# Kernel optimization log

Hardware: AMD Instinct MI355X
Metric: run time of the kernel (lower is better)

## Reference

```python
import jax, jax.numpy as jnp
import numpy as np

B, T, N, D = 256, 200, 8, 64
MODEL = N * D          # 512
FFN_H = 1024 * N // 4  # 2048
EPS = 1.1920929e-07    # torch.finfo(float32).eps (nn.RMSNorm default eps=None)


def setup_inputs() -> dict:
    key = jax.random.key(0)
    ks = jax.random.split(key, 9)
    def xavier(k, shape):
        fan_in, fan_out = shape[-2], shape[-1]
        lim = float(np.sqrt(6.0 / (fan_in + fan_out)))
        return jax.random.uniform(k, shape, jnp.float32, -lim, lim)
    q = jax.random.normal(ks[0], (B, N, D), jnp.float32)
    seq = jax.random.normal(ks[1], (B, T, MODEL), jnp.float32)
    seq_mask = jax.random.randint(ks[2], (B, T), 0, 2) > 0
    seq_mask = seq_mask.at[:, 0].set(True)  # ensure >=1 valid position per row
    return {
        "q": q,
        "seq": seq,
        "rms_w": jnp.ones((MODEL,), jnp.float32),
        "w1": xavier(ks[3], (MODEL, FFN_H)),
        "w2": xavier(ks[4], (MODEL, FFN_H)),
        "w3": xavier(ks[5], (FFN_H, MODEL)),
        "w_k": xavier(ks[6], (N, D, D)),
        "w_v": xavier(ks[7], (N, D, D)),
        "seq_mask": seq_mask,
    }


def reference(q, seq, rms_w, w1, w2, w3, w_k, w_v, seq_mask):
    # RMSNorm
    sn = seq * jax.lax.rsqrt(jnp.mean(seq * seq, axis=-1, keepdims=True) + EPS) * rms_w
    # SwiGLU FFN + residual (dropout=0 / eval)
    h = (jax.nn.silu(sn @ w1) * (sn @ w2)) @ w3 + seq  # (B,T,N*D)
    hh = h.reshape(B, T, N, D)
    keys = jnp.einsum('btnd,nde->bnte', hh, w_k)    # (B,N,T,D)
    values = jnp.einsum('btnd,nde->bnte', hh, w_v)  # (B,N,T,D)
    scale = D ** (-0.5)
    scores = jnp.einsum('bnd,bntd->bnt', q, keys) * scale  # single-query attention
    scores = jnp.where(seq_mask[:, None, :], scores, -jnp.inf)
    attn = jax.nn.softmax(scores, axis=-1)
    ctx = jnp.einsum('bnt,bntd->bnd', attn, values)
    return ctx + q
```

## Files before the change

### kernel.cpp

```cpp
#include <hip/hip_runtime.h>
#include <hip/hip_fp16.h>
#include <cstdint>
#include <cstddef>

typedef unsigned short u16t;
typedef __bf16 bf16x8 __attribute__((ext_vector_type(8)));
typedef float f32x4 __attribute__((ext_vector_type(4)));
typedef unsigned short u16x8 __attribute__((ext_vector_type(8)));

#define BT_ROWS 51200
#define MODEL 512
#define FFNH 2048

__device__ __forceinline__ float bf2f(u16t u) {
  union { unsigned int i; float f; } v; v.i = ((unsigned int)u) << 16; return v.f;
}
__device__ __forceinline__ u16t f2bf(float f) {
  union { float f; unsigned int i; } v; v.f = f;
  return (u16t)((v.i + 0x7fffu + ((v.i >> 16) & 1u)) >> 16);
}
__device__ __forceinline__ float ldf(const void* p, size_t i, int dt) {
  if (dt == 1) return ((const float*)p)[i];
  u16t u = ((const u16t*)p)[i];
  if (dt == 0) return bf2f(u);
  __half h; *(u16t*)&h = u; return __half2float(h);
}
__device__ __forceinline__ void stf(void* p, size_t i, int dt, float f) {
  if (dt == 1) { ((float*)p)[i] = f; }
  else if (dt == 0) { ((u16t*)p)[i] = f2bf(f); }
  else { __half h = __float2half(f); ((u16t*)p)[i] = *(u16t*)&h; }
}
__device__ __forceinline__ void gl2lds16(const void* g, void* l) {
  __builtin_amdgcn_global_load_lds((const __attribute__((address_space(1))) void*)g,
                                   (__attribute__((address_space(3))) void*)l, 16, 0, 0);
}

__global__ __launch_bounds__(256) void detect_dtype_k(const unsigned int* __restrict__ w1,
                                                      int* __restrict__ dflag) {
  __shared__ int sh[8];
  int a = 0, bc = 0;
  for (int it = 0; it < 64; it++) {
    unsigned int w = w1[it * 256 + threadIdx.x];
    u16t lo = (u16t)(w & 0xffffu), hi = (u16t)(w >> 16);
    float flo = bf2f(lo);
    a += (!(fabsf(flo) < 0.25f)) ? 1 : 0;
    __half hh; *(u16t*)&hh = hi; float fhi = __half2float(hh);
    bc += (fabsf(fhi) > 0.25f && fabsf(fhi) < 256.f) ? 1 : 0;
  }
#pragma unroll
  for (int o = 32; o; o >>= 1) { a += __shfl_xor(a, o); bc += __shfl_xor(bc, o); }
  int w = threadIdx.x >> 6;
  if ((threadIdx.x & 63) == 0) { sh[w] = a; sh[4 + w] = bc; }
  __syncthreads();
  if (threadIdx.x == 0) {
    int A = sh[0] + sh[1] + sh[2] + sh[3];
    int B = sh[4] + sh[5] + sh[6] + sh[7];
    dflag[0] = (A > 256) ? 1 : ((B < 256) ? 2 : 0);
  }
}

__global__ __launch_bounds__(256) void detect_mask_k(const unsigned int* __restrict__ msk,
                                                     int* __restrict__ flag) {
  int i = blockIdx.x * 256 + threadIdx.x;
  int bad = 0;
  if (i < 12800) bad = (msk[i] > 1u) ? 1 : 0;
  unsigned long long bl = __ballot(bad);
  if ((threadIdx.x & 63) == 0 && bl) atomicOr(flag, 1);
}

__global__ __launch_bounds__(256) void rmsnorm_k(const void* __restrict__ seq,
                                                 const void* __restrict__ w,
                                                 const int* __restrict__ dfp,
                                                 u16t* __restrict__ xn) {
  const int dt = dfp[0];
  int row = blockIdx.x * 4 + (threadIdx.x >> 6);
  int lane = threadIdx.x & 63;
  size_t base = (size_t)row * MODEL + lane * 8;
  float x[8]; float ss = 0.f;
  if (dt == 0) {
    u16x8 xv = *(const u16x8*)((const u16t*)seq + base);
#pragma unroll
    for (int j = 0; j < 8; j++) { x[j] = bf2f(xv[j]); ss += x[j] * x[j]; }
  } else if (dt == 1) {
    const f32x4* p = (const f32x4*)((const float*)seq + base);
    f32x4 va = p[0], vb = p[1];
#pragma unroll
    for (int j = 0; j < 4; j++) { x[j] = va[j]; x[4 + j] = vb[j]; }
#pragma unroll
    for (int j = 0; j < 8; j++) ss += x[j] * x[j];
  } else {
#pragma unroll
    for (int j = 0; j < 8; j++) { x[j] = ldf(seq, base + j, dt); ss += x[j] * x[j]; }
  }
#pragma unroll
  for (int o = 32; o; o >>= 1) ss += __shfl_xor(ss, o);
  float rstd = rsqrtf(ss * (1.f / 512.f) + 1.1920929e-07f);
  u16x8 ov;
#pragma unroll
  for (int j = 0; j < 8; j++) ov[j] = f2bf(x[j] * rstd * ldf(w, lane * 8 + j, dt));
  *(u16x8*)(xn + base) = ov;
}

__global__ __launch_bounds__(256) void transpose_k(const void* __restrict__ src,
                                                   u16t* __restrict__ dst,
                                                   const int* __restrict__ dfp,
                                                   int R, int C) {
  const int dt = dfp[0];
  __shared__ u16t tile[32][33];
  int x = threadIdx.x & 31, y = threadIdx.x >> 5;
  int c0 = blockIdx.x * 32, r0 = blockIdx.y * 32;
#pragma unroll
  for (int i = 0; i < 32; i += 8)
    tile[y + i][x] = f2bf(ldf(src, (size_t)(r0 + y + i) * C + c0 + x, dt));
  __syncthreads();
#pragma unroll
  for (int i = 0; i < 32; i += 8) dst[(size_t)(c0 + y + i) * R + r0 + x] = tile[x][y + i];
}


__global__ __launch_bounds__(256, 4) void ffn_gemm1(const u16t* __restrict__ Xn,
                                                    const u16t* __restrict__ W1t,
                                                    const u16t* __restrict__ W2t,
                                                    u16t* __restrict__ Act) {
  __shared__ u16t As[128 * 64];
  __shared__ u16t B1s[64 * 64];
  __shared__ u16t B2s[64 * 64];
  const int tid = threadIdx.x;
  const int lane = tid & 63;
  const int wave = tid >> 6;
  const int wr = wave >> 1, wc = wave & 1;
  const int quad = lane >> 4, l16 = lane & 15;
  const int nBase = blockIdx.x * 64;
  const int mBase = blockIdx.y * 128;
  const int wuBase = tid & ~63;

  f32x4 acc1[4][2], acc2[4][2];
  const f32x4 zf = {0.f, 0.f, 0.f, 0.f};
#pragma unroll
  for (int i = 0; i < 4; i++)
#pragma unroll
    for (int j = 0; j < 2; j++) { acc1[i][j] = zf; acc2[i][j] = zf; }

  for (int kt = 0; kt < MODEL; kt += 64) {
#pragma unroll
    for (int c = 0; c < 4; c++) {
      int chunk = c * 256 + tid;
      int r = chunk >> 3, k8 = (chunk & 7) ^ (r & 7);
      gl2lds16(Xn + (size_t)(mBase + r) * MODEL + kt + k8 * 8, As + (size_t)(c * 256 + wuBase) * 8);
    }
#pragma unroll
    for (int c = 0; c < 2; c++) {
      int chunk = c * 256 + tid;
      int r = chunk >> 3, k8 = (chunk & 7) ^ (r & 7);
      gl2lds16(W1t + (size_t)(nBase + r) * MODEL + kt + k8 * 8, B1s + (size_t)(c * 256 + wuBase) * 8);
      gl2lds16(W2t + (size_t)(nBase + r) * MODEL + kt + k8 * 8, B2s + (size_t)(c * 256 + wuBase) * 8);
    }
    __syncthreads();
#pragma unroll
    for (int ks = 0; ks < 64; ks += 32) {
      bf16x8 a[4], b1[2], b2[2];
      const int sw = (ks >> 3) + quad;
#pragma unroll
      for (int mi = 0; mi < 4; mi++) {
        int row = wr * 64 + mi * 16 + l16;
        a[mi] = *(const bf16x8*)(As + row * 64 + ((sw ^ (row & 7)) << 3));
      }
#pragma unroll
      for (int ni = 0; ni < 2; ni++) {
        int row = wc * 32 + ni * 16 + l16;
        b1[ni] = *(const bf16x8*)(B1s + row * 64 + ((sw ^ (row & 7)) << 3));
        b2[ni] = *(const bf16x8*)(B2s + row * 64 + ((sw ^ (row & 7)) << 3));
      }
#pragma unroll
      for (int mi = 0; mi < 4; mi++)
#pragma unroll
        for (int ni = 0; ni < 2; ni++) {
          acc1[mi][ni] = __builtin_amdgcn_mfma_f32_16x16x32_bf16(a[mi], b1[ni], acc1[mi][ni], 0, 0, 0);
          acc2[mi][ni] = __builtin_amdgcn_mfma_f32_16x16x32_bf16(a[mi], b2[ni], acc2[mi][ni], 0, 0, 0);
        }
    }
    __syncthreads();
  }
#pragma unroll
  for (int mi = 0; mi < 4; mi++)
#pragma unroll
    for (int ni = 0; ni < 2; ni++)
#pragma unroll
      for (int r = 0; r < 4; r++) {
        int row = mBase + wr * 64 + mi * 16 + quad * 4 + r;
        int col = nBase + wc * 32 + ni * 16 + l16;
        float g1 = acc1[mi][ni][r], g2 = acc2[mi][ni][r];
        float sl = g1 / (1.f + __expf(-g1));
        Act[(size_t)row * FFNH + col] = f2bf(sl * g2);
      }
}

__global__ __launch_bounds__(256, 4) void ffn_gemm2(const u16t* __restrict__ Act,
                                                    const u16t* __restrict__ W3t,
                                                    const void* __restrict__ Seq,
                                                    const int* __restrict__ dfp,
                                                    u16t* __restrict__ H, int rowOff) {
  __shared__ u16t As[128 * 64];
  __shared__ u16t Bs[128 * 64];
  const int dt = dfp[0];
  const int tid = threadIdx.x;
  const int lane = tid & 63;
  const int wave = tid >> 6;
  const int wr = wave >> 1, wc = wave & 1;
  const int quad = lane >> 4, l16 = lane & 15;
  const int nBase = blockIdx.x * 128;
  const int mBase = blockIdx.y * 128;
  const int wuBase = tid & ~63;

  f32x4 acc[4][4];
  const f32x4 zf = {0.f, 0.f, 0.f, 0.f};
#pragma unroll
  for (int i = 0; i < 4; i++)
#pragma unroll
    for (int j = 0; j < 4; j++) acc[i][j] = zf;

  for (int kt = 0; kt < FFNH; kt += 64) {
#pragma unroll
    for (int c = 0; c < 4; c++) {
      int chunk = c * 256 + tid;
      int r = chunk >> 3, k8 = (chunk & 7) ^ (r & 7);
      gl2lds16(Act + (size_t)(mBase + r) * FFNH + kt + k8 * 8, As + (size_t)(c * 256 + wuBase) * 8);
      gl2lds16(W3t + (size_t)(nBase + r) * FFNH + kt + k8 * 8, Bs + (size_t)(c * 256 + wuBase) * 8);
    }
    __syncthreads();
#pragma unroll
    for (int ks = 0; ks < 64; ks += 32) {
      bf16x8 a[4], b[4];
      const int sw = (ks >> 3) + quad;
#pragma unroll
      for (int mi = 0; mi < 4; mi++) {
        int row = wr * 64 + mi * 16 + l16;
        a[mi] = *(const bf16x8*)(As + row * 64 + ((sw ^ (row & 7)) << 3));
      }
#pragma unroll
      for (int ni = 0; ni < 4; ni++) {
        int row = wc * 64 + ni * 16 + l16;
        b[ni] = *(const bf16x8*)(Bs + row * 64 + ((sw ^ (row & 7)) << 3));
      }
#pragma unroll
      for (int mi = 0; mi < 4; mi++)
#pragma unroll
        for (int ni = 0; ni < 4; ni++)
          acc[mi][ni] = __builtin_amdgcn_mfma_f32_16x16x32_bf16(a[mi], b[ni], acc[mi][ni], 0, 0, 0);
    }
    __syncthreads();
  }
#pragma unroll
  for (int mi = 0; mi < 4; mi++)
#pragma unroll
    for (int ni = 0; ni < 4; ni++)
#pragma unroll
      for (int r = 0; r < 4; r++) {
        int grow = rowOff + mBase + wr * 64 + mi * 16 + quad * 4 + r;
        int col = nBase + wc * 64 + ni * 16 + l16;
        float v = acc[mi][ni][r] + ldf(Seq, (size_t)grow * MODEL + col, dt);
        H[(size_t)grow * MODEL + col] = f2bf(v);
      }
}

__global__ __launch_bounds__(256) void attn_k(const u16t* __restrict__ H,
                                              const void* __restrict__ q,
                                              const void* __restrict__ wk,
                                              const void* __restrict__ wv,
                                              const int* __restrict__ mask,
                                              const int* __restrict__ mflagp,
                                              const int* __restrict__ dfp,
                                              void* __restrict__ out) {
  const int b = blockIdx.x >> 3;
  const int n = blockIdx.x & 7;
  const int tid = threadIdx.x;
  const int w = tid >> 6;
  const int lane = tid & 63;
  const int T = 200;
  const int HS = 66;
  const int dt = dfp[0];
  const int mflag = mflagp[0];

  __shared__ u16t hbuf[200 * HS];
  __shared__ float qk[64];
  __shared__ float sc[200];
  __shared__ float part[256];
  __shared__ float red[8];
  __shared__ float ctx[64];

  for (int chunk = tid; chunk < 1600; chunk += 256) {
    int r = chunk >> 3, c = (chunk & 7) << 3;
    u16x8 v = *(const u16x8*)(H + (size_t)(b * 200 + r) * MODEL + n * 64 + c);
#pragma unroll
    for (int j = 0; j < 8; j++) hbuf[r * HS + c + j] = v[j];
  }

  {
    int d = tid >> 2, sub = tid & 3;
    float s = 0.f;
    size_t wb = ((size_t)n * 64 + d) * 64 + sub * 16;
    size_t qb = (size_t)(b * 8 + n) * 64 + sub * 16;
#pragma unroll
    for (int i = 0; i < 16; i++) s += ldf(wk, wb + i, dt) * ldf(q, qb + i, dt);
    part[tid] = s;
  }
  __syncthreads();
  if (tid < 64) qk[tid] = part[tid * 4] + part[tid * 4 + 1] + part[tid * 4 + 2] + part[tid * 4 + 3];
  __syncthreads();

  float sv = -INFINITY;
  if (tid < T) {
    float s = 0.f;
#pragma unroll 16
    for (int d = 0; d < 64; d++) s += bf2f(hbuf[tid * HS + d]) * qk[d];
    int mv = mflag ? (int)((const unsigned char*)mask)[b * 200 + tid] : mask[b * 200 + tid];
    sv = mv ? s * 0.125f : -INFINITY;
  }

  float mx = sv;
#pragma unroll
  for (int o = 32; o; o >>= 1) mx = fmaxf(mx, __shfl_xor(mx, o));
  if (lane == 0) red[w] = mx;
  __syncthreads();
  float gmax = fmaxf(fmaxf(red[0], red[1]), fmaxf(red[2], red[3]));
  float e = 0.f;
  if (gmax == -INFINITY) {
    if (tid == 0) e = 1.f;
  } else if (tid < T) {
    e = __expf(sv - gmax);
  }
  float s = e;
#pragma unroll
  for (int o = 32; o; o >>= 1) s += __shfl_xor(s, o);
  if (lane == 0) red[4 + w] = s;
  __syncthreads();
  float inv = 1.f / (red[4] + red[5] + red[6] + red[7]);
  if (tid < T) sc[tid] = e * inv;
  __syncthreads();

  float a2 = 0.f;
  for (int t = w; t < T; t += 4) a2 += sc[t] * bf2f(hbuf[t * HS + lane]);
  part[tid] = a2;
  __syncthreads();
  if (tid < 64) ctx[tid] = part[tid] + part[64 + tid] + part[128 + tid] + part[192 + tid];
  __syncthreads();

  {
    int od = tid & 63;
    float s2 = 0.f;
#pragma unroll
    for (int i = 0; i < 16; i++) {
      int d = w * 16 + i;
      s2 += ctx[d] * ldf(wv, ((size_t)n * 64 + d) * 64 + od, dt);
    }
    part[tid] = s2;
  }
  __syncthreads();
  if (tid < 64) {
    size_t oi = (size_t)(b * 8 + n) * 64 + tid;
    stf(out, oi, dt,
        part[tid] + part[64 + tid] + part[128 + tid] + part[192 + tid] + ldf(q, oi, dt));
  }
}

extern "C" void kernel_launch(void* const* d_in, const int* in_sizes, int n_in,
                              void* d_out, int out_size, void* d_ws, size_t ws_size,
                              hipStream_t stream) {
  (void)in_sizes; (void)n_in; (void)out_size;
  const void* q   = d_in[0];
  const void* seq = d_in[1];
  const void* rw  = d_in[2];
  const void* w1  = d_in[3];
  const void* w2  = d_in[4];
  const void* w3  = d_in[5];
  const void* wk  = d_in[6];
  const void* wv  = d_in[7];
  const int*  msk = (const int*)d_in[8];

  char* ws = (char*)d_ws;
  size_t off = 0;
  auto alloc = [&](size_t b) { void* p = ws + off; off = (off + b + 255) & ~(size_t)255; return p; };
  int*  flags = (int*)alloc(512);
  int*  mflag = flags + 0;
  int*  dflag = flags + 4;
  u16t* Xn  = (u16t*)alloc((size_t)BT_ROWS * MODEL * 2);
  u16t* W1t = (u16t*)alloc((size_t)FFNH * MODEL * 2);
  u16t* W2t = (u16t*)alloc((size_t)FFNH * MODEL * 2);
  u16t* W3t = (u16t*)alloc((size_t)MODEL * FFNH * 2);
  size_t actBytes = (ws_size > off) ? (ws_size - off) : 0;
  long tpc = (long)(actBytes / ((size_t)128 * FFNH * 2));
  if (tpc < 1) tpc = 1;
  if (tpc > 200) tpc = 200;
  u16t* ActB = (u16t*)(ws + off);

  hipMemsetAsync(flags, 0, 512, stream);
  detect_dtype_k<<<dim3(1), dim3(256), 0, stream>>>((const unsigned int*)w1, dflag);
  detect_mask_k<<<dim3(50), dim3(256), 0, stream>>>((const unsigned int*)msk, mflag);

  rmsnorm_k<<<dim3(BT_ROWS / 4), dim3(256), 0, stream>>>(seq, rw, dflag, Xn);
  transpose_k<<<dim3(FFNH / 32, MODEL / 32), dim3(256), 0, stream>>>(w1, W1t, dflag, MODEL, FFNH);
  transpose_k<<<dim3(FFNH / 32, MODEL / 32), dim3(256), 0, stream>>>(w2, W2t, dflag, MODEL, FFNH);
  transpose_k<<<dim3(MODEL / 32, FFNH / 32), dim3(256), 0, stream>>>(w3, W3t, dflag, FFNH, MODEL);

  for (int t0 = 0; t0 < 400; t0 += (int)tpc) {
    int tiles = (400 - t0 < (int)tpc) ? (400 - t0) : (int)tpc;
    int rows0 = t0 * 128;
    ffn_gemm1<<<dim3(FFNH / 64, tiles), dim3(256), 0, stream>>>(
        Xn + (size_t)rows0 * MODEL, W1t, W2t, ActB);
    ffn_gemm2<<<dim3(MODEL / 128, tiles), dim3(256), 0, stream>>>(
        ActB, W3t, seq, dflag, Xn, rows0);
  }
  attn_k<<<dim3(2048), dim3(256), 0, stream>>>(Xn, q, wk, wv, msk, mflag, dflag, d_out);
}
```

Baseline: 693.5 us.

## Rewrite FFN GEMMs as 256x256 tiles with software-pipelined LDS double buffering

Both FFN GEMMs move from 128-row tiles on 256 threads to 256x256 tiles on 512 threads. A shared gemm256_core double-buffers the LDS stages and interleaves global-to-LDS loads with MFMA quarter-blocks, using explicit vmcnt waits, sched barriers and setprio. W1 and W2 are transposed into one interleaved buffer so a single B tile carries matching gate and up columns for the SwiGLU epilogue, and block indices are swizzled across XCDs for L2 locality. This targets LDS/global traffic and barrier stalls, at the cost of higher register and LDS pressure and fewer resident blocks per CU.

```diff
diff --git a/kernel.cpp b/kernel.cpp
--- a/kernel.cpp
+++ b/kernel.cpp
@@ -104,7 +104,7 @@
 __global__ __launch_bounds__(256) void transpose_k(const void* __restrict__ src,
                                                    u16t* __restrict__ dst,
                                                    const int* __restrict__ dfp,
-                                                   int R, int C) {
+                                                   int R, int C, int ih) {
   const int dt = dfp[0];
   __shared__ u16t tile[32][33];
   int x = threadIdx.x & 31, y = threadIdx.x >> 5;
@@ -114,150 +114,203 @@
     tile[y + i][x] = f2bf(ldf(src, (size_t)(r0 + y + i) * C + c0 + x, dt));
   __syncthreads();
 #pragma unroll
-  for (int i = 0; i < 32; i += 8) dst[(size_t)(c0 + y + i) * R + r0 + x] = tile[x][y + i];
-}
-
-
-__global__ __launch_bounds__(256, 4) void ffn_gemm1(const u16t* __restrict__ Xn,
-                                                    const u16t* __restrict__ W1t,
-                                                    const u16t* __restrict__ W2t,
-                                                    u16t* __restrict__ Act) {
-  __shared__ u16t As[128 * 64];
-  __shared__ u16t B1s[64 * 64];
-  __shared__ u16t B2s[64 * 64];
+  for (int i = 0; i < 32; i += 8) {
+    int n = c0 + y + i;
+    int vr = (ih >= 0) ? (((n >> 4) << 5) + ih * 16 + (n & 15)) : n;
+    dst[(size_t)vr * R + r0 + x] = tile[x][y + i];
+  }
+}
+
+
+#define FENCE_BAR()                              \
+  do {                                           \
+    __builtin_amdgcn_sched_barrier(0);           \
+    __builtin_amdgcn_s_barrier();                \
+    __builtin_amdgcn_sched_barrier(0);           \
+  } while (0)
+
+#define MM16(afr, bfr, MHc, NHc)                                                    \
+  do {                                                                              \
+    __builtin_amdgcn_s_setprio(1);                                                  \
+    _Pragma("unroll") for (int ks_ = 0; ks_ < 2; ks_++)                             \
+        _Pragma("unroll") for (int mi_ = 0; mi_ < 4; mi_++)                         \
+            _Pragma("unroll") for (int ni_ = 0; ni_ < 2; ni_++)                     \
+                acc[(MHc)*4 + mi_][(NHc)*2 + ni_] =                                 \
+                    __builtin_amdgcn_mfma_f32_16x16x32_bf16(                        \
+                        afr[mi_][ks_], bfr[ni_][ks_],                               \
+                        acc[(MHc)*4 + mi_][(NHc)*2 + ni_], 0, 0, 0);                \
+    __builtin_amdgcn_s_setprio(0);                                                  \
+  } while (0)
+
+template <int K>
+__device__ __forceinline__ void gemm256_core(const u16t* __restrict__ Ag,
+                                             const u16t* __restrict__ Bg,
+                                             u16t* __restrict__ As,
+                                             u16t* __restrict__ Bs,
+                                             f32x4 (&acc)[8][4]) {
+  constexpr int NKT = K / 64;
   const int tid = threadIdx.x;
   const int lane = tid & 63;
   const int wave = tid >> 6;
-  const int wr = wave >> 1, wc = wave & 1;
+  const int wr = wave >> 2, wc = wave & 3;
   const int quad = lane >> 4, l16 = lane & 15;
-  const int nBase = blockIdx.x * 64;
-  const int mBase = blockIdx.y * 128;
-  const int wuBase = tid & ~63;
-
-  f32x4 acc1[4][2], acc2[4][2];
+  const int wu = tid & ~63;
+
+  auto stage = [&](const u16t* __restrict__ G, u16t* __restrict__ L, int s, int h) {
+#pragma unroll
+    for (int c = 0; c < 2; c++) {
+      int chunk = c * 512 + tid;
+      int r = chunk >> 3;
+      int k8 = (chunk & 7) ^ (r & 7);
+      gl2lds16(G + (size_t)(h * 128 + r) * K + s * 64 + k8 * 8,
+               L + (s & 1) * 16384 + h * 8192 + (size_t)(c * 512 + wu) * 8);
+    }
+  };
+  auto lda = [&](bf16x8(&a)[4][2], int u, int MH) {
+    const u16t* S = As + (u & 1) * 16384;
+#pragma unroll
+    for (int ks = 0; ks < 2; ks++)
+#pragma unroll
+      for (int mi = 0; mi < 4; mi++) {
+        int row = wr * 128 + MH * 64 + mi * 16 + l16;
+        int sw = (ks * 4 + quad) ^ (row & 7);
+        a[mi][ks] = *(const bf16x8*)(S + row * 64 + sw * 8);
+      }
+  };
+  auto ldb = [&](bf16x8(&b)[2][2], int u, int NH) {
+    const u16t* S = Bs + (u & 1) * 16384;
+#pragma unroll
+    for (int ks = 0; ks < 2; ks++)
+#pragma unroll
+      for (int ni = 0; ni < 2; ni++) {
+        int row = wc * 64 + NH * 32 + ni * 16 + l16;
+        int sw = (ks * 4 + quad) ^ (row & 7);
+        b[ni][ks] = *(const bf16x8*)(S + row * 64 + sw * 8);
+      }
+  };
+
+  bf16x8 a[4][2], b0[2][2], b1[2][2];
+
+  stage(Ag, As, 0, 0);
+  stage(Ag, As, 0, 1);
+  stage(Bg, Bs, 0, 0);
+  stage(Bg, Bs, 0, 1);
+  if (NKT > 1) stage(Ag, As, 1, 0);
+  __builtin_amdgcn_sched_barrier(0);
+  if (NKT > 1) asm volatile("s_waitcnt vmcnt(2)" ::: "memory");
+  else         asm volatile("s_waitcnt vmcnt(0)" ::: "memory");
+  __builtin_amdgcn_s_barrier();
+  __builtin_amdgcn_sched_barrier(0);
+
+  for (int u = 0; u < NKT; u++) {
+    lda(a, u, 0);
+    ldb(b0, u, 0);
+    if (u + 1 < NKT) stage(Ag, As, u + 1, 1);
+    FENCE_BAR();
+    MM16(a, b0, 0, 0);
+    FENCE_BAR();
+    ldb(b1, u, 1);
+    if (u + 1 < NKT) stage(Bg, Bs, u + 1, 0);
+    FENCE_BAR();
+    MM16(a, b1, 0, 1);
+    FENCE_BAR();
+    lda(a, u, 1);
+    if (u + 1 < NKT) stage(Bg, Bs, u + 1, 1);
+    FENCE_BAR();
+    MM16(a, b0, 1, 0);
+    FENCE_BAR();
+    if (u + 2 < NKT) stage(Ag, As, u + 2, 0);
+    FENCE_BAR();
+    MM16(a, b1, 1, 1);
+    __builtin_amdgcn_sched_barrier(0);
+    if (u < NKT - 2)       asm volatile("s_waitcnt vmcnt(2)" ::: "memory");
+    else if (u == NKT - 2) asm volatile("s_waitcnt vmcnt(0)" ::: "memory");
+    __builtin_amdgcn_s_barrier();
+    __builtin_amdgcn_sched_barrier(0);
+  }
+}
+
+__device__ __forceinline__ int xcd_swz(int o, int nwg) {
+  int q = nwg >> 3, r = nwg & 7;
+  int xcd = o & 7, i = o >> 3;
+  return (xcd < r ? xcd * (q + 1) : r * (q + 1) + (xcd - r) * q) + i;
+}
+
+__global__ __launch_bounds__(512, 2) void ffn_gemm1(const u16t* __restrict__ Xn,
+                                                    const u16t* __restrict__ W12t,
+                                                    u16t* __restrict__ Act) {
+  __shared__ u16t As[2 * 16384];
+  __shared__ u16t Bs[2 * 16384];
+  const int tid = threadIdx.x;
+  const int lane = tid & 63;
+  const int wave = tid >> 6;
+  const int wr = wave >> 2, wc = wave & 3;
+  const int quad = lane >> 4, l16 = lane & 15;
+
+  int o = blockIdx.y * 16 + blockIdx.x;
+  int s = xcd_swz(o, gridDim.y * 16);
+  int bx = s & 15, by = s >> 4;
+
+  f32x4 acc[8][4];
   const f32x4 zf = {0.f, 0.f, 0.f, 0.f};
 #pragma unroll
-  for (int i = 0; i < 4; i++)
-#pragma unroll
-    for (int j = 0; j < 2; j++) { acc1[i][j] = zf; acc2[i][j] = zf; }
-
-  for (int kt = 0; kt < MODEL; kt += 64) {
-#pragma unroll
-    for (int c = 0; c < 4; c++) {
-      int chunk = c * 256 + tid;
-      int r = chunk >> 3, k8 = (chunk & 7) ^ (r & 7);
-      gl2lds16(Xn + (size_t)(mBase + r) * MODEL + kt + k8 * 8, As + (size_t)(c * 256 + wuBase) * 8);
-    }
-#pragma unroll
-    for (int c = 0; c < 2; c++) {
-      int chunk = c * 256 + tid;
-      int r = chunk >> 3, k8 = (chunk & 7) ^ (r & 7);
-      gl2lds16(W1t + (size_t)(nBase + r) * MODEL + kt + k8 * 8, B1s + (size_t)(c * 256 + wuBase) * 8);
-      gl2lds16(W2t + (size_t)(nBase + r) * MODEL + kt + k8 * 8, B2s + (size_t)(c * 256 + wuBase) * 8);
-    }
-    __syncthreads();
-#pragma unroll
-    for (int ks = 0; ks < 64; ks += 32) {
-      bf16x8 a[4], b1[2], b2[2];
-      const int sw = (ks >> 3) + quad;
-#pragma unroll
-      for (int mi = 0; mi < 4; mi++) {
-        int row = wr * 64 + mi * 16 + l16;
-        a[mi] = *(const bf16x8*)(As + row * 64 + ((sw ^ (row & 7)) << 3));
-      }
-#pragma unroll
-      for (int ni = 0; ni < 2; ni++) {
-        int row = wc * 32 + ni * 16 + l16;
-        b1[ni] = *(const bf16x8*)(B1s + row * 64 + ((sw ^ (row & 7)) << 3));
-        b2[ni] = *(const bf16x8*)(B2s + row * 64 + ((sw ^ (row & 7)) << 3));
-      }
-#pragma unroll
-      for (int mi = 0; mi < 4; mi++)
-#pragma unroll
-        for (int ni = 0; ni < 2; ni++) {
-          acc1[mi][ni] = __builtin_amdgcn_mfma_f32_16x16x32_bf16(a[mi], b1[ni], acc1[mi][ni], 0, 0, 0);
-          acc2[mi][ni] = __builtin_amdgcn_mfma_f32_16x16x32_bf16(a[mi], b2[ni], acc2[mi][ni], 0, 0, 0);
-        }
-    }
-    __syncthreads();
-  }
-#pragma unroll
-  for (int mi = 0; mi < 4; mi++)
-#pragma unroll
-    for (int ni = 0; ni < 2; ni++)
+  for (int m = 0; m < 8; m++)
+#pragma unroll
+    for (int n = 0; n < 4; n++) acc[m][n] = zf;
+
+  gemm256_core<512>(Xn + (size_t)by * 256 * 512, W12t + (size_t)bx * 256 * 512, As, Bs, acc);
+
+  const int mBase = by * 256;
+#pragma unroll
+  for (int mi = 0; mi < 8; mi++)
+#pragma unroll
+    for (int p = 0; p < 2; p++)
 #pragma unroll
       for (int r = 0; r < 4; r++) {
-        int row = mBase + wr * 64 + mi * 16 + quad * 4 + r;
-        int col = nBase + wc * 32 + ni * 16 + l16;
-        float g1 = acc1[mi][ni][r], g2 = acc2[mi][ni][r];
+        int row = mBase + wr * 128 + mi * 16 + quad * 4 + r;
+        int col = bx * 128 + (wc * 2 + p) * 16 + l16;
+        float g1 = acc[mi][2 * p][r], g2 = acc[mi][2 * p + 1][r];
         float sl = g1 / (1.f + __expf(-g1));
         Act[(size_t)row * FFNH + col] = f2bf(sl * g2);
       }
 }
 
-__global__ __launch_bounds__(256, 4) void ffn_gemm2(const u16t* __restrict__ Act,
+__global__ __launch_bounds__(512, 2) void ffn_gemm2(const u16t* __restrict__ Act,
                                                     const u16t* __restrict__ W3t,
                                                     const void* __restrict__ Seq,
                                                     const int* __restrict__ dfp,
                                                     u16t* __restrict__ H, int rowOff) {
-  __shared__ u16t As[128 * 64];
-  __shared__ u16t Bs[128 * 64];
+  __shared__ u16t As[2 * 16384];
+  __shared__ u16t Bs[2 * 16384];
   const int dt = dfp[0];
   const int tid = threadIdx.x;
   const int lane = tid & 63;
   const int wave = tid >> 6;
-  const int wr = wave >> 1, wc = wave & 1;
+  const int wr = wave >> 2, wc = wave & 3;
   const int quad = lane >> 4, l16 = lane & 15;
-  const int nBase = blockIdx.x * 128;
-  const int mBase = blockIdx.y * 128;
-  const int wuBase = tid & ~63;
-
-  f32x4 acc[4][4];
+
+  int o = blockIdx.y * 2 + blockIdx.x;
+  int s = xcd_swz(o, gridDim.y * 2);
+  int bx = s & 1, by = s >> 1;
+
+  f32x4 acc[8][4];
   const f32x4 zf = {0.f, 0.f, 0.f, 0.f};
 #pragma unroll
-  for (int i = 0; i < 4; i++)
-#pragma unroll
-    for (int j = 0; j < 4; j++) acc[i][j] = zf;
-
-  for (int kt = 0; kt < FFNH; kt += 64) {
-#pragma unroll
-    for (int c = 0; c < 4; c++) {
-      int chunk = c * 256 + tid;
-      int r = chunk >> 3, k8 = (chunk & 7) ^ (r & 7);
-      gl2lds16(Act + (size_t)(mBase + r) * FFNH + kt + k8 * 8, As + (size_t)(c * 256 + wuBase) * 8);
-      gl2lds16(W3t + (size_t)(nBase + r) * FFNH + kt + k8 * 8, Bs + (size_t)(c * 256 + wuBase) * 8);
-    }
-    __syncthreads();
-#pragma unroll
-    for (int ks = 0; ks < 64; ks += 32) {
-      bf16x8 a[4], b[4];
-      const int sw = (ks >> 3) + quad;
-#pragma unroll
-      for (int mi = 0; mi < 4; mi++) {
-        int row = wr * 64 + mi * 16 + l16;
-        a[mi] = *(const bf16x8*)(As + row * 64 + ((sw ^ (row & 7)) << 3));
-      }
-#pragma unroll
-      for (int ni = 0; ni < 4; ni++) {
-        int row = wc * 64 + ni * 16 + l16;
-        b[ni] = *(const bf16x8*)(Bs + row * 64 + ((sw ^ (row & 7)) << 3));
-      }
-#pragma unroll
-      for (int mi = 0; mi < 4; mi++)
-#pragma unroll
-        for (int ni = 0; ni < 4; ni++)
-          acc[mi][ni] = __builtin_amdgcn_mfma_f32_16x16x32_bf16(a[mi], b[ni], acc[mi][ni], 0, 0, 0);
-    }
-    __syncthreads();
-  }
-#pragma unroll
-  for (int mi = 0; mi < 4; mi++)
+  for (int m = 0; m < 8; m++)
+#pragma unroll
+    for (int n = 0; n < 4; n++) acc[m][n] = zf;
+
+  gemm256_core<2048>(Act + (size_t)by * 256 * 2048, W3t + (size_t)bx * 256 * 2048, As, Bs, acc);
+
+  const int mBase = by * 256;
+#pragma unroll
+  for (int mi = 0; mi < 8; mi++)
 #pragma unroll
     for (int ni = 0; ni < 4; ni++)
 #pragma unroll
       for (int r = 0; r < 4; r++) {
-        int grow = rowOff + mBase + wr * 64 + mi * 16 + quad * 4 + r;
-        int col = nBase + wc * 64 + ni * 16 + l16;
+        int grow = rowOff + mBase + wr * 128 + mi * 16 + quad * 4 + r;
+        int col = bx * 256 + wc * 64 + ni * 16 + l16;
         float v = acc[mi][ni][r] + ldf(Seq, (size_t)grow * MODEL + col, dt);
         H[(size_t)grow * MODEL + col] = f2bf(v);
       }
@@ -383,14 +436,13 @@
   int*  flags = (int*)alloc(512);
   int*  mflag = flags + 0;
   int*  dflag = flags + 4;
-  u16t* Xn  = (u16t*)alloc((size_t)BT_ROWS * MODEL * 2);
-  u16t* W1t = (u16t*)alloc((size_t)FFNH * MODEL * 2);
-  u16t* W2t = (u16t*)alloc((size_t)FFNH * MODEL * 2);
-  u16t* W3t = (u16t*)alloc((size_t)MODEL * FFNH * 2);
+  u16t* Xn   = (u16t*)alloc((size_t)BT_ROWS * MODEL * 2);
+  u16t* W12t = (u16t*)alloc((size_t)2 * FFNH * MODEL * 2);
+  u16t* W3t  = (u16t*)alloc((size_t)MODEL * FFNH * 2);
   size_t actBytes = (ws_size > off) ? (ws_size - off) : 0;
-  long tpc = (long)(actBytes / ((size_t)128 * FFNH * 2));
-  if (tpc < 1) tpc = 1;
-  if (tpc > 200) tpc = 200;
+  long ppc = (long)(actBytes / ((size_t)256 * FFNH * 2));
+  if (ppc < 1) ppc = 1;
+  if (ppc > 100) ppc = 100;
   u16t* ActB = (u16t*)(ws + off);
 
   hipMemsetAsync(flags, 0, 512, stream);
@@ -398,16 +450,16 @@
   detect_mask_k<<<dim3(50), dim3(256), 0, stream>>>((const unsigned int*)msk, mflag);
 
   rmsnorm_k<<<dim3(BT_ROWS / 4), dim3(256), 0, stream>>>(seq, rw, dflag, Xn);
-  transpose_k<<<dim3(FFNH / 32, MODEL / 32), dim3(256), 0, stream>>>(w1, W1t, dflag, MODEL, FFNH);
-  transpose_k<<<dim3(FFNH / 32, MODEL / 32), dim3(256), 0, stream>>>(w2, W2t, dflag, MODEL, FFNH);
-  transpose_k<<<dim3(MODEL / 32, FFNH / 32), dim3(256), 0, stream>>>(w3, W3t, dflag, FFNH, MODEL);
-
-  for (int t0 = 0; t0 < 400; t0 += (int)tpc) {
-    int tiles = (400 - t0 < (int)tpc) ? (400 - t0) : (int)tpc;
-    int rows0 = t0 * 128;
-    ffn_gemm1<<<dim3(FFNH / 64, tiles), dim3(256), 0, stream>>>(
-        Xn + (size_t)rows0 * MODEL, W1t, W2t, ActB);
-    ffn_gemm2<<<dim3(MODEL / 128, tiles), dim3(256), 0, stream>>>(
+  transpose_k<<<dim3(FFNH / 32, MODEL / 32), dim3(256), 0, stream>>>(w1, W12t, dflag, MODEL, FFNH, 0);
+  transpose_k<<<dim3(FFNH / 32, MODEL / 32), dim3(256), 0, stream>>>(w2, W12t, dflag, MODEL, FFNH, 1);
+  transpose_k<<<dim3(MODEL / 32, FFNH / 32), dim3(256), 0, stream>>>(w3, W3t, dflag, FFNH, MODEL, -1);
+
+  for (int p0 = 0; p0 < 200; p0 += (int)ppc) {
+    int panels = (200 - p0 < (int)ppc) ? (200 - p0) : (int)ppc;
+    int rows0 = p0 * 256;
+    ffn_gemm1<<<dim3(16, panels), dim3(512), 0, stream>>>(
+        Xn + (size_t)rows0 * MODEL, W12t, ActB);
+    ffn_gemm2<<<dim3(2, panels), dim3(512), 0, stream>>>(
         ActB, W3t, seq, dflag, Xn, rows0);
   }
   attn_k<<<dim3(2048), dim3(256), 0, stream>>>(Xn, q, wk, wv, msk, mflag, dflag, d_out);
```

After: 774.7 us. 1.12x slower.

## Stage gemm1 epilogue through LDS and widen gemm2 tiles to 128x256

Applied to the files above, without the earlier changes.

The first FFN GEMM now writes its SiLU-gated output into shared memory and then stores it with 16-byte vectorised global writes, instead of scattered 2-byte stores. The second GEMM doubles its output tile width to 256 columns, with each wave owning a 128x64 sub-tile. This halves the grid and the number of times the activation tiles are reloaded. The cost is more accumulators per thread and lower occupancy (launch bounds 2 instead of 4), which could hurt latency hiding.

```diff
diff --git a/kernel.cpp b/kernel.cpp
--- a/kernel.cpp
+++ b/kernel.cpp
@@ -122,9 +122,10 @@
                                                     const u16t* __restrict__ W1t,
                                                     const u16t* __restrict__ W2t,
                                                     u16t* __restrict__ Act) {
-  __shared__ u16t As[128 * 64];
-  __shared__ u16t B1s[64 * 64];
-  __shared__ u16t B2s[64 * 64];
+  __shared__ u16t shs[16384];
+  u16t* As  = shs;
+  u16t* B1s = shs + 8192;
+  u16t* B2s = shs + 12288;
   const int tid = threadIdx.x;
   const int lane = tid & 63;
   const int wave = tid >> 6;
@@ -187,35 +188,42 @@
     for (int ni = 0; ni < 2; ni++)
 #pragma unroll
       for (int r = 0; r < 4; r++) {
-        int row = mBase + wr * 64 + mi * 16 + quad * 4 + r;
-        int col = nBase + wc * 32 + ni * 16 + l16;
+        int rl = wr * 64 + mi * 16 + quad * 4 + r;
+        int cl = wc * 32 + ni * 16 + l16;
         float g1 = acc1[mi][ni][r], g2 = acc2[mi][ni][r];
         float sl = g1 / (1.f + __expf(-g1));
-        Act[(size_t)row * FFNH + col] = f2bf(sl * g2);
-      }
-}
-
-__global__ __launch_bounds__(256, 4) void ffn_gemm2(const u16t* __restrict__ Act,
+        shs[rl * 72 + cl] = f2bf(sl * g2);
+      }
+  __syncthreads();
+  {
+    int row = tid >> 1, half = tid & 1;
+    const u16t* sp = shs + row * 72 + half * 32;
+    u16t* gp = Act + (size_t)(mBase + row) * FFNH + nBase + half * 32;
+#pragma unroll
+    for (int j = 0; j < 4; j++) *(u16x8*)(gp + j * 8) = *(const u16x8*)(sp + j * 8);
+  }
+}
+
+__global__ __launch_bounds__(256, 2) void ffn_gemm2(const u16t* __restrict__ Act,
                                                     const u16t* __restrict__ W3t,
                                                     const void* __restrict__ Seq,
                                                     const int* __restrict__ dfp,
                                                     u16t* __restrict__ H, int rowOff) {
   __shared__ u16t As[128 * 64];
-  __shared__ u16t Bs[128 * 64];
+  __shared__ u16t Bs[256 * 64];
   const int dt = dfp[0];
   const int tid = threadIdx.x;
   const int lane = tid & 63;
-  const int wave = tid >> 6;
-  const int wr = wave >> 1, wc = wave & 1;
+  const int wc = tid >> 6;
   const int quad = lane >> 4, l16 = lane & 15;
-  const int nBase = blockIdx.x * 128;
+  const int nBase = blockIdx.x * 256;
   const int mBase = blockIdx.y * 128;
   const int wuBase = tid & ~63;
 
-  f32x4 acc[4][4];
+  f32x4 acc[8][4];
   const f32x4 zf = {0.f, 0.f, 0.f, 0.f};
 #pragma unroll
-  for (int i = 0; i < 4; i++)
+  for (int i = 0; i < 8; i++)
 #pragma unroll
     for (int j = 0; j < 4; j++) acc[i][j] = zf;
 
@@ -225,16 +233,21 @@
       int chunk = c * 256 + tid;
       int r = chunk >> 3, k8 = (chunk & 7) ^ (r & 7);
       gl2lds16(Act + (size_t)(mBase + r) * FFNH + kt + k8 * 8, As + (size_t)(c * 256 + wuBase) * 8);
+    }
+#pragma unroll
+    for (int c = 0; c < 8; c++) {
+      int chunk = c * 256 + tid;
+      int r = chunk >> 3, k8 = (chunk & 7) ^ (r & 7);
       gl2lds16(W3t + (size_t)(nBase + r) * FFNH + kt + k8 * 8, Bs + (size_t)(c * 256 + wuBase) * 8);
     }
     __syncthreads();
 #pragma unroll
     for (int ks = 0; ks < 64; ks += 32) {
-      bf16x8 a[4], b[4];
+      bf16x8 a[8], b[4];
       const int sw = (ks >> 3) + quad;
 #pragma unroll
-      for (int mi = 0; mi < 4; mi++) {
-        int row = wr * 64 + mi * 16 + l16;
+      for (int mi = 0; mi < 8; mi++) {
+        int row = mi * 16 + l16;
         a[mi] = *(const bf16x8*)(As + row * 64 + ((sw ^ (row & 7)) << 3));
       }
 #pragma unroll
@@ -243,7 +256,7 @@
         b[ni] = *(const bf16x8*)(Bs + row * 64 + ((sw ^ (row & 7)) << 3));
       }
 #pragma unroll
-      for (int mi = 0; mi < 4; mi++)
+      for (int mi = 0; mi < 8; mi++)
 #pragma unroll
         for (int ni = 0; ni < 4; ni++)
           acc[mi][ni] = __builtin_amdgcn_mfma_f32_16x16x32_bf16(a[mi], b[ni], acc[mi][ni], 0, 0, 0);
@@ -251,12 +264,12 @@
     __syncthreads();
   }
 #pragma unroll
-  for (int mi = 0; mi < 4; mi++)
+  for (int mi = 0; mi < 8; mi++)
 #pragma unroll
     for (int ni = 0; ni < 4; ni++)
 #pragma unroll
       for (int r = 0; r < 4; r++) {
-        int grow = rowOff + mBase + wr * 64 + mi * 16 + quad * 4 + r;
+        int grow = rowOff + mBase + mi * 16 + quad * 4 + r;
         int col = nBase + wc * 64 + ni * 16 + l16;
         float v = acc[mi][ni][r] + ldf(Seq, (size_t)grow * MODEL + col, dt);
         H[(size_t)grow * MODEL + col] = f2bf(v);
@@ -407,7 +420,7 @@
     int rows0 = t0 * 128;
     ffn_gemm1<<<dim3(FFNH / 64, tiles), dim3(256), 0, stream>>>(
         Xn + (size_t)rows0 * MODEL, W1t, W2t, ActB);
-    ffn_gemm2<<<dim3(MODEL / 128, tiles), dim3(256), 0, stream>>>(
+    ffn_gemm2<<<dim3(MODEL / 256, tiles), dim3(256), 0, stream>>>(
         ActB, W3t, seq, dflag, Xn, rows0);
   }
   attn_k<<<dim3(2048), dim3(256), 0, stream>>>(Xn, q, wk, wv, msk, mflag, dflag, d_out);
```

Result: slower. 738.6 us (+6.5%).

## Inline dtype detection, merge weight transposes, and swizzle GEMM block order

Applied to the files above, without the earlier changes.

Removes the separate dtype-detect kernel and memset by having each kernel detect the dtype from a wavefront-wide ballot over 64 words of w1. The mask check is collapsed to a single block, and the three transpose launches become one. A block-index swizzle is added to both FFN GEMMs to improve cache locality. Together these aim to cut launch count and serialization overhead. The risk is that the reduced dtype-detection sample is less robust than the original heuristic.

```diff
diff --git a/kernel.cpp b/kernel.cpp
--- a/kernel.cpp
+++ b/kernel.cpp
@@ -35,44 +35,46 @@
                                    (__attribute__((address_space(3))) void*)l, 16, 0, 0);
 }
 
-__global__ __launch_bounds__(256) void detect_dtype_k(const unsigned int* __restrict__ w1,
-                                                      int* __restrict__ dflag) {
-  __shared__ int sh[8];
-  int a = 0, bc = 0;
-  for (int it = 0; it < 64; it++) {
-    unsigned int w = w1[it * 256 + threadIdx.x];
-    u16t lo = (u16t)(w & 0xffffu), hi = (u16t)(w >> 16);
-    float flo = bf2f(lo);
-    a += (!(fabsf(flo) < 0.25f)) ? 1 : 0;
-    __half hh; *(u16t*)&hh = hi; float fhi = __half2float(hh);
-    bc += (fabsf(fhi) > 0.25f && fabsf(fhi) < 256.f) ? 1 : 0;
-  }
-#pragma unroll
-  for (int o = 32; o; o >>= 1) { a += __shfl_xor(a, o); bc += __shfl_xor(bc, o); }
-  int w = threadIdx.x >> 6;
-  if ((threadIdx.x & 63) == 0) { sh[w] = a; sh[4 + w] = bc; }
-  __syncthreads();
-  if (threadIdx.x == 0) {
-    int A = sh[0] + sh[1] + sh[2] + sh[3];
-    int B = sh[4] + sh[5] + sh[6] + sh[7];
-    dflag[0] = (A > 256) ? 1 : ((B < 256) ? 2 : 0);
-  }
+__device__ __forceinline__ int detect_dt_inline(const unsigned int* __restrict__ w1p) {
+  int lane = threadIdx.x & 63;
+  unsigned int w = w1p[lane];
+  u16t lo = (u16t)(w & 0xffffu), hi = (u16t)(w >> 16);
+  float flo = bf2f(lo);
+  __half hh; *(u16t*)&hh = hi; float fhi = __half2float(hh);
+  int afire = (!(fabsf(flo) < 0.25f)) ? 1 : 0;
+  int bfire = (fabsf(fhi) > 0.25f && fabsf(fhi) < 256.f) ? 1 : 0;
+  int A = __popcll(__ballot(afire));
+  int B = __popcll(__ballot(bfire));
+  return (A > 16) ? 1 : ((B < 16) ? 2 : 0);
+}
+
+__device__ __forceinline__ void swz_xy(int& bx, int& by, const int NX) {
+  int NY = gridDim.y;
+  if ((NY & 3) != 0) return;
+  int lid = by * NX + bx;
+  int k = lid & 7, j = lid >> 3;
+  const int hx = NX >> 1;
+  bx = (k & 1) * hx + (j % hx);
+  by = (k >> 1) * (NY >> 2) + (j / hx);
 }
 
 __global__ __launch_bounds__(256) void detect_mask_k(const unsigned int* __restrict__ msk,
                                                      int* __restrict__ flag) {
-  int i = blockIdx.x * 256 + threadIdx.x;
+  __shared__ int sh[4];
   int bad = 0;
-  if (i < 12800) bad = (msk[i] > 1u) ? 1 : 0;
+  for (int it = 0; it < 50; it++) bad |= (msk[it * 256 + threadIdx.x] > 1u) ? 1 : 0;
   unsigned long long bl = __ballot(bad);
-  if ((threadIdx.x & 63) == 0 && bl) atomicOr(flag, 1);
+  int w = threadIdx.x >> 6;
+  if ((threadIdx.x & 63) == 0) sh[w] = (bl != 0ull) ? 1 : 0;
+  __syncthreads();
+  if (threadIdx.x == 0) flag[0] = sh[0] | sh[1] | sh[2] | sh[3];
 }
 
 __global__ __launch_bounds__(256) void rmsnorm_k(const void* __restrict__ seq,
                                                  const void* __restrict__ w,
-                                                 const int* __restrict__ dfp,
+                                                 const unsigned int* __restrict__ w1p,
                                                  u16t* __restrict__ xn) {
-  const int dt = dfp[0];
+  const int dt = detect_dt_inline(w1p);
   int row = blockIdx.x * 4 + (threadIdx.x >> 6);
   int lane = threadIdx.x & 63;
   size_t base = (size_t)row * MODEL + lane * 8;
@@ -101,14 +103,21 @@
   *(u16x8*)(xn + base) = ov;
 }
 
-__global__ __launch_bounds__(256) void transpose_k(const void* __restrict__ src,
-                                                   u16t* __restrict__ dst,
-                                                   const int* __restrict__ dfp,
-                                                   int R, int C) {
-  const int dt = dfp[0];
+__global__ __launch_bounds__(256) void transpose3_k(const void* __restrict__ w1,
+                                                    const void* __restrict__ w2,
+                                                    const void* __restrict__ w3,
+                                                    u16t* __restrict__ W1t,
+                                                    u16t* __restrict__ W2t,
+                                                    u16t* __restrict__ W3t) {
+  const int dt = detect_dt_inline((const unsigned int*)w1);
   __shared__ u16t tile[32][33];
+  int bid = blockIdx.x;
+  const void* src; u16t* dst; int R, C, bx, by;
+  if (bid < 1024)      { src = w1; dst = W1t; R = MODEL; C = FFNH; bx = bid & 63; by = bid >> 6; }
+  else if (bid < 2048) { int t = bid - 1024; src = w2; dst = W2t; R = MODEL; C = FFNH; bx = t & 63; by = t >> 6; }
+  else                 { int t = bid - 2048; src = w3; dst = W3t; R = FFNH; C = MODEL; bx = t & 15; by = t >> 4; }
   int x = threadIdx.x & 31, y = threadIdx.x >> 5;
-  int c0 = blockIdx.x * 32, r0 = blockIdx.y * 32;
+  int c0 = bx * 32, r0 = by * 32;
 #pragma unroll
   for (int i = 0; i < 32; i += 8)
     tile[y + i][x] = f2bf(ldf(src, (size_t)(r0 + y + i) * C + c0 + x, dt));
@@ -130,8 +139,10 @@
   const int wave = tid >> 6;
   const int wr = wave >> 1, wc = wave & 1;
   const int quad = lane >> 4, l16 = lane & 15;
-  const int nBase = blockIdx.x * 64;
-  const int mBase = blockIdx.y * 128;
+  int bx = blockIdx.x, by = blockIdx.y;
+  swz_xy(bx, by, 32);
+  const int nBase = bx * 64;
+  const int mBase = by * 128;
   const int wuBase = tid & ~63;
 
   f32x4 acc1[4][2], acc2[4][2];
@@ -198,18 +209,20 @@
 __global__ __launch_bounds__(256, 4) void ffn_gemm2(const u16t* __restrict__ Act,
                                                     const u16t* __restrict__ W3t,
                                                     const void* __restrict__ Seq,
-                                                    const int* __restrict__ dfp,
+                                                    const unsigned int* __restrict__ w1p,
                                                     u16t* __restrict__ H, int rowOff) {
   __shared__ u16t As[128 * 64];
   __shared__ u16t Bs[128 * 64];
-  const int dt = dfp[0];
+  const int dt = detect_dt_inline(w1p);
   const int tid = threadIdx.x;
   const int lane = tid & 63;
   const int wave = tid >> 6;
   const int wr = wave >> 1, wc = wave & 1;
   const int quad = lane >> 4, l16 = lane & 15;
-  const int nBase = blockIdx.x * 128;
-  const int mBase = blockIdx.y * 128;
+  int bx = blockIdx.x, by = blockIdx.y;
+  swz_xy(bx, by, 4);
+  const int nBase = bx * 128;
+  const int mBase = by * 128;
   const int wuBase = tid & ~63;
 
   f32x4 acc[4][4];
@@ -269,7 +282,7 @@
                                               const void* __restrict__ wv,
                                               const int* __restrict__ mask,
                                               const int* __restrict__ mflagp,
-                                              const int* __restrict__ dfp,
+                                              const unsigned int* __restrict__ w1p,
                                               void* __restrict__ out) {
   const int b = blockIdx.x >> 3;
   const int n = blockIdx.x & 7;
@@ -278,7 +291,7 @@
   const int lane = tid & 63;
   const int T = 200;
   const int HS = 66;
-  const int dt = dfp[0];
+  const int dt = detect_dt_inline(w1p);
   const int mflag = mflagp[0];
 
   __shared__ u16t hbuf[200 * HS];
@@ -382,7 +395,6 @@
   auto alloc = [&](size_t b) { void* p = ws + off; off = (off + b + 255) & ~(size_t)255; return p; };
   int*  flags = (int*)alloc(512);
   int*  mflag = flags + 0;
-  int*  dflag = flags + 4;
   u16t* Xn  = (u16t*)alloc((size_t)BT_ROWS * MODEL * 2);
   u16t* W1t = (u16t*)alloc((size_t)FFNH * MODEL * 2);
   u16t* W2t = (u16t*)alloc((size_t)FFNH * MODEL * 2);
@@ -393,14 +405,9 @@
   if (tpc > 200) tpc = 200;
   u16t* ActB = (u16t*)(ws + off);
 
-  hipMemsetAsync(flags, 0, 512, stream);
-  detect_dtype_k<<<dim3(1), dim3(256), 0, stream>>>((const unsigned int*)w1, dflag);
-  detect_mask_k<<<dim3(50), dim3(256), 0, stream>>>((const unsigned int*)msk, mflag);
-
-  rmsnorm_k<<<dim3(BT_ROWS / 4), dim3(256), 0, stream>>>(seq, rw, dflag, Xn);
-  transpose_k<<<dim3(FFNH / 32, MODEL / 32), dim3(256), 0, stream>>>(w1, W1t, dflag, MODEL, FFNH);
-  transpose_k<<<dim3(FFNH / 32, MODEL / 32), dim3(256), 0, stream>>>(w2, W2t, dflag, MODEL, FFNH);
-  transpose_k<<<dim3(MODEL / 32, FFNH / 32), dim3(256), 0, stream>>>(w3, W3t, dflag, FFNH, MODEL);
+  detect_mask_k<<<dim3(1), dim3(256), 0, stream>>>((const unsigned int*)msk, mflag);
+  rmsnorm_k<<<dim3(BT_ROWS / 4), dim3(256), 0, stream>>>(seq, rw, (const unsigned int*)w1, Xn);
+  transpose3_k<<<dim3(3072), dim3(256), 0, stream>>>(w1, w2, w3, W1t, W2t, W3t);
 
   for (int t0 = 0; t0 < 400; t0 += (int)tpc) {
     int tiles = (400 - t0 < (int)tpc) ? (400 - t0) : (int)tpc;
@@ -408,7 +415,8 @@
     ffn_gemm1<<<dim3(FFNH / 64, tiles), dim3(256), 0, stream>>>(
         Xn + (size_t)rows0 * MODEL, W1t, W2t, ActB);
     ffn_gemm2<<<dim3(MODEL / 128, tiles), dim3(256), 0, stream>>>(
-        ActB, W3t, seq, dflag, Xn, rows0);
-  }
-  attn_k<<<dim3(2048), dim3(256), 0, stream>>>(Xn, q, wk, wv, msk, mflag, dflag, d_out);
-}
+        ActB, W3t, seq, (const unsigned int*)w1, Xn, rows0);
+  }
+  attn_k<<<dim3(2048), dim3(256), 0, stream>>>(Xn, q, wk, wv, msk, mflag,
+                                               (const unsigned int*)w1, d_out);
+}
```

Result: faster. 634.4 us (-8.5%).
